# Kernel tuning notes

Hardware: AMD Instinct MI355X
Metric: run time of the kernel (lower is better)

## Reference

```python
import jax, jax.numpy as jnp
import numpy as np

NUM_GRAPHS = 10  # seq_len graphs batched together


def _gat_layer(x, W, al, ar, b, src, dst, n_nodes):
    # x: [N, h_dim]; W: [h_dim, H*D]; al/ar/b: [H, D]
    H, D = al.shape
    feat = (x @ W).reshape(-1, H, D)                      # [N, H, D]
    el = jnp.einsum('nhd,hd->nh', feat, al)               # [N, H]
    er = jnp.einsum('nhd,hd->nh', feat, ar)               # [N, H]
    e = jax.nn.leaky_relu(el[src] + er[dst], 0.2)         # [E, H]
    # edge softmax over incoming edges of each dst node (stable)
    emax = jax.ops.segment_max(e, dst, num_segments=n_nodes)
    emax = jnp.where(jnp.isfinite(emax), emax, 0.0)
    w = jnp.exp(e - emax[dst])                            # [E, H]
    denom = jax.ops.segment_sum(w, dst, num_segments=n_nodes)  # [N, H]
    msg = w[:, :, None] * feat[src]                       # [E, H, D]
    agg = jax.ops.segment_sum(msg, dst, num_segments=n_nodes)  # [N, H, D]
    out = agg / jnp.maximum(denom, 1e-9)[:, :, None] + b
    return out.mean(axis=1)                               # [N, h_dim] (mean over heads)


def setup_inputs() -> dict:
    key = jax.random.key(0)
    ks = jax.random.split(key, 16)
    N, E, V, h, H = 100000, 1000000, 50000, 64, 3
    node_ids = jax.random.randint(ks[0], (N,), 0, V)
    edge_src = jax.random.randint(ks[1], (E,), 0, N)
    edge_dst = jax.random.randint(ks[2], (E,), 0, N)
    node_graph_id = jnp.sort(jax.random.randint(ks[3], (N,), 0, NUM_GRAPHS))
    s = 1.0 / np.sqrt(h)
    return {
        'node_ids': node_ids, 'edge_src': edge_src, 'edge_dst': edge_dst,
        'node_graph_id': node_graph_id,
        'W_embed': jax.random.normal(ks[4], (V, h), jnp.float32),
        'W1': jax.random.normal(ks[5], (h, H * h), jnp.float32) * s,
        'al1': jax.random.normal(ks[6], (H, h), jnp.float32) * s,
        'ar1': jax.random.normal(ks[7], (H, h), jnp.float32) * s,
        'b1': jnp.zeros((H, h), jnp.float32),
        'W2': jax.random.normal(ks[8], (h, H * h), jnp.float32) * s,
        'al2': jax.random.normal(ks[9], (H, h), jnp.float32) * s,
        'ar2': jax.random.normal(ks[10], (H, h), jnp.float32) * s,
        'b2': jnp.zeros((H, h), jnp.float32),
    }


def reference(node_ids, edge_src, edge_dst, node_graph_id, W_embed,
              W1, al1, ar1, b1, W2, al2, ar2, b2):
    n_nodes = node_ids.shape[0]
    h = W_embed[node_ids]                                 # gather embeddings
    h = _gat_layer(h, W1, al1, ar1, b1, edge_src, edge_dst, n_nodes)
    h = _gat_layer(h, W2, al2, ar2, b2, edge_src, edge_dst, n_nodes)
    # dgl.max_nodes: per-graph max pooling over nodes
    global_info = jax.ops.segment_max(h, node_graph_id, num_segments=NUM_GRAPHS)
    return global_info                                    # [NUM_GRAPHS, h_dim]
```

## Files before the change

kernel.cpp:

```cpp
#include <hip/hip_runtime.h>
#include <math.h>


#define HEADS 3
#define HD 64
#define FDIM (HEADS*HD)
#define NCOL 208
#define NUM_GRAPHS 10
#define NPB 32

typedef short bf16x8 __attribute__((ext_vector_type(8)));
typedef float f32x4  __attribute__((ext_vector_type(4)));

__device__ __forceinline__ float bf2f(unsigned short u) {
    return __uint_as_float(((unsigned int)u) << 16);
}
__device__ __forceinline__ unsigned short f2bf(float f) {
    unsigned int u = __float_as_uint(f);
    unsigned int r = (u + 0x7FFFu + ((u >> 16) & 1u)) >> 16;
    return (unsigned short)r;
}

__device__ __forceinline__ int wave_incl_scan(int v, int lane) {
#pragma unroll
    for (int off = 1; off < 64; off <<= 1) {
        int t = __shfl_up(v, off);
        if (lane >= off) v += t;
    }
    return v;
}

__device__ __forceinline__ unsigned int fmap(float f) {
    unsigned int u = __float_as_uint(f);
    return (u & 0x80000000u) ? ~u : (u | 0x80000000u);
}
__device__ __forceinline__ float funmap(unsigned int u) {
    u = (u & 0x80000000u) ? (u & 0x7FFFFFFFu) : ~u;
    return __uint_as_float(u);
}

__global__ void k_prep(const float* __restrict__ W1, const float* __restrict__ al1,
                       const float* __restrict__ ar1,
                       const float* __restrict__ W2, const float* __restrict__ al2,
                       const float* __restrict__ ar2,
                       unsigned short* __restrict__ Wt1, unsigned short* __restrict__ Wt2,
                       unsigned int* __restrict__ gm) {
    int i = blockIdx.x * blockDim.x + threadIdx.x;
    if (i < 2 * NCOL * HD) {
        int l = i / (NCOL * HD), j = i % (NCOL * HD);
        int c = j >> 6, k = j & 63;
        const float* W  = l ? W2  : W1;
        const float* al = l ? al2 : al1;
        const float* ar = l ? ar2 : ar1;
        unsigned short* Wt = l ? Wt2 : Wt1;
        float v = 0.f;
        if (c < FDIM) {
            v = W[k * FDIM + c];
        } else if (c < FDIM + 6) {
            int h = c - FDIM;
            const float* a = (h < 3) ? al : ar;
            int hh = (h < 3) ? h : h - 3;
            float s = 0.f;
            for (int d = 0; d < HD; ++d)
                s += W[k * FDIM + hh * HD + d] * a[hh * HD + d];
            v = s;
        }
        Wt[j] = f2bf(v);
    }
    if (i < NUM_GRAPHS * HD) gm[i] = 0x007FFFFFu;
}

__global__ void k_hist(const int* __restrict__ dst, int* __restrict__ deg, int E) {
    int i = blockIdx.x * blockDim.x + threadIdx.x;
    if (i < E) atomicAdd(&deg[dst[i]], 1);
}

__global__ void k_scan1(const int* __restrict__ deg, int* __restrict__ tmp,
                        int* __restrict__ partials, int N) {
    int t = threadIdx.x, b = blockIdx.x;
    int i = b * 256 + t;
    int v = (i < N) ? deg[i] : 0;
    int lane = t & 63, w = t >> 6;
    int incl = wave_incl_scan(v, lane);
    __shared__ int wsum[4];
    if (lane == 63) wsum[w] = incl;
    __syncthreads();
    int off = 0;
    for (int j = 0; j < w; ++j) off += wsum[j];
    incl += off;
    if (i < N) tmp[i] = incl;
    if (t == 255) partials[b] = incl;
}

__global__ void k_scan2(int* __restrict__ partials, int nb) {
    int t = threadIdx.x;
    int v = (t < nb) ? partials[t] : 0;
    int lane = t & 63, w = t >> 6;
    int incl = wave_incl_scan(v, lane);
    __shared__ int wsum[8];
    if (lane == 63) wsum[w] = incl;
    __syncthreads();
    int off = 0;
    for (int j = 0; j < w; ++j) off += wsum[j];
    incl += off;
    if (t < nb) partials[t] = incl;
}

__global__ void k_scan3(const int* __restrict__ tmp, const int* __restrict__ deg,
                        const int* __restrict__ partials, int* __restrict__ rowptr,
                        int* __restrict__ cur, int N) {
    int i = blockIdx.x * blockDim.x + threadIdx.x;
    if (i >= N) return;
    int b = i >> 8;
    int off = b ? partials[b - 1] : 0;
    int incl = tmp[i] + off;
    rowptr[i + 1] = incl;
    cur[i] = incl - deg[i];
    if (i == 0) rowptr[0] = 0;
}

__global__ void k_scatter(const int* __restrict__ src, const int* __restrict__ dst,
                          int* __restrict__ cur, int* __restrict__ csrc, int E) {
    int i = blockIdx.x * blockDim.x + threadIdx.x;
    if (i >= E) return;
    int pos = atomicAdd(&cur[dst[i]], 1);
    csrc[pos] = src[i];
}

__global__ __launch_bounds__(256) void k_feat_mfma(
        const unsigned short* __restrict__ xbf, const int* __restrict__ ids,
        const float* __restrict__ Wemb, const unsigned short* __restrict__ Wt,
        unsigned short* __restrict__ feat, float4* __restrict__ el4,
        float4* __restrict__ er4, int N) {
    __shared__ unsigned short xs[NPB][72];
    __shared__ unsigned short ls[NPB][200];
    int t = threadIdx.x;
    int lane = t & 63, w = t >> 6;
    int base = blockIdx.x * NPB;

    if (ids) {
        for (int i = t; i < NPB * 16; i += 256) {
            int row = i >> 4, c4 = (i & 15) * 4;
            int n = base + row;
            float4 v = {0.f, 0.f, 0.f, 0.f};
            if (n < N) v = *(const float4*)(Wemb + (size_t)ids[n] * HD + c4);
            unsigned short* dp = &xs[row][c4];
            dp[0] = f2bf(v.x); dp[1] = f2bf(v.y); dp[2] = f2bf(v.z); dp[3] = f2bf(v.w);
        }
    } else {
        for (int i = t; i < NPB * 16; i += 256) {
            int row = i >> 4, c4 = (i & 15) * 4;
            int n = base + row;
            ushort4 v = {0, 0, 0, 0};
            if (n < N) v = *(const ushort4*)(xbf + (size_t)n * HD + c4);
            *(ushort4*)(&xs[row][c4]) = v;
        }
    }

    int ntile = (w == 3) ? 4 : 3;
    bf16x8 bfrag[4][2];
#pragma unroll
    for (int c = 0; c < 4; ++c) {
        if (c >= ntile) break;
#pragma unroll
        for (int kk = 0; kk < 2; ++kk) {
            int coln = (w * 3 + c) * 16 + (lane & 15);
            int k0 = kk * 32 + (lane >> 4) * 8;
            bfrag[c][kk] = *(const bf16x8*)(Wt + (size_t)coln * HD + k0);
        }
    }
    __syncthreads();

    f32x4 acc[2][4];
#pragma unroll
    for (int r = 0; r < 2; ++r)
#pragma unroll
        for (int c = 0; c < 4; ++c) acc[r][c] = (f32x4){0.f, 0.f, 0.f, 0.f};
#pragma unroll
    for (int r = 0; r < 2; ++r)
#pragma unroll
        for (int kk = 0; kk < 2; ++kk) {
            int row = r * 16 + (lane & 15);
            int k0 = kk * 32 + (lane >> 4) * 8;
            bf16x8 a = *(const bf16x8*)(&xs[row][k0]);
#pragma unroll
            for (int c = 0; c < 4; ++c) {
                if (c >= ntile) break;
                acc[r][c] = __builtin_amdgcn_mfma_f32_16x16x32_bf16(a, bfrag[c][kk], acc[r][c], 0, 0, 0);
            }
        }

#pragma unroll
    for (int r = 0; r < 2; ++r)
#pragma unroll
        for (int c = 0; c < 3; ++c) {
            int col = (w * 3 + c) * 16 + (lane & 15);
#pragma unroll
            for (int j = 0; j < 4; ++j) {
                int row = r * 16 + (lane >> 4) * 4 + j;
                ls[row][col] = f2bf(acc[r][c][j]);
            }
        }

    if (w == 3) {
        int col = lane & 15;
        if (col < 6) {
#pragma unroll
            for (int r = 0; r < 2; ++r)
#pragma unroll
                for (int j = 0; j < 4; ++j) {
                    int row = r * 16 + (lane >> 4) * 4 + j;
                    int n = base + row;
                    if (n < N) {
                        float v = acc[r][3][j];
                        if (col < 3) ((float*)&el4[n])[col] = v;
                        else         ((float*)&er4[n])[col - 3] = v;
                    }
                }
        }
    }
    __syncthreads();

    for (int i = t; i < NPB * FDIM / 4; i += 256) {
        int idx = i * 4;
        int row = idx / FDIM, col = idx % FDIM;
        int n = base + row;
        if (n < N)
            *(ushort4*)(feat + (size_t)n * FDIM + col) = *(const ushort4*)(&ls[row][col]);
    }
}

__global__ void k_gather(const int* __restrict__ rowptr, const int* __restrict__ csrc,
                         const float4* __restrict__ el4, const float4* __restrict__ er4,
                         const unsigned short* __restrict__ feat,
                         const float* __restrict__ b,
                         unsigned short* __restrict__ xout, int N) {
    __shared__ float4 stage[4][64];
    int wid = (blockIdx.x * blockDim.x + threadIdx.x) >> 6;
    int lane = threadIdx.x & 63, w = (threadIdx.x >> 6) & 3;
    if (wid >= N) return;
    int beg = rowptr[wid], end = rowptr[wid + 1];
    int deg = end - beg;
    float4 er = er4[wid];
    float acc0 = 0.f, acc1 = 0.f, acc2 = 0.f;
    float ds0 = 0.f, ds1 = 0.f, ds2 = 0.f;
    for (int cb = 0; cb < deg; cb += 64) {
        int nch = min(64, deg - cb);
        if (lane < nch) {
            int s = csrc[beg + cb + lane];
            float4 l = el4[s];
            float e0 = l.x + er.x; e0 = e0 >= 0.f ? e0 : 0.2f * e0;
            float e1 = l.y + er.y; e1 = e1 >= 0.f ? e1 : 0.2f * e1;
            float e2 = l.z + er.z; e2 = e2 >= 0.f ? e2 : 0.2f * e2;
            float4 o;
            o.x = __int_as_float(s);
            o.y = __expf(e0); o.z = __expf(e1); o.w = __expf(e2);
            stage[w][lane] = o;
        }
        __builtin_amdgcn_wave_barrier();
#pragma unroll 4
        for (int j = 0; j < nch; ++j) {
            float4 e = stage[w][j];
            int s = __float_as_int(e.x);
            const unsigned short* frow = feat + (size_t)s * FDIM;
            acc0 = fmaf(e.y, bf2f(frow[lane]), acc0);
            acc1 = fmaf(e.z, bf2f(frow[HD + lane]), acc1);
            acc2 = fmaf(e.w, bf2f(frow[2 * HD + lane]), acc2);
            ds0 += e.y; ds1 += e.z; ds2 += e.w;
        }
        __builtin_amdgcn_wave_barrier();
    }
    float o = (acc0 / fmaxf(ds0, 1e-9f) + b[lane])
            + (acc1 / fmaxf(ds1, 1e-9f) + b[HD + lane])
            + (acc2 / fmaxf(ds2, 1e-9f) + b[2 * HD + lane]);
    xout[(size_t)wid * HD + lane] = f2bf(o * (1.f / 3.f));
}

__global__ void k_gmax(const unsigned short* __restrict__ x, const int* __restrict__ gid,
                       unsigned int* __restrict__ gm, int N) {
    int lane = threadIdx.x;
    int base = blockIdx.x * 64;
    int endn = min(base + 64, N);
    int cur = -1;
    float m = 0.f;
    for (int n = base; n < endn; ++n) {
        int g = gid[n];
        float v = bf2f(x[(size_t)n * HD + lane]);
        if (g != cur) {
            if (cur >= 0) atomicMax(&gm[cur * HD + lane], fmap(m));
            cur = g; m = v;
        } else {
            m = fmaxf(m, v);
        }
    }
    if (cur >= 0) atomicMax(&gm[cur * HD + lane], fmap(m));
}

__global__ void k_gmax_final(const unsigned int* __restrict__ gm, float* __restrict__ out) {
    int i = blockIdx.x * blockDim.x + threadIdx.x;
    if (i < NUM_GRAPHS * HD) out[i] = funmap(gm[i]);
}

extern "C" void kernel_launch(void* const* d_in, const int* in_sizes, int n_in,
                              void* d_out, int out_size, void* d_ws, size_t ws_size,
                              hipStream_t stream) {
    const int*   node_ids = (const int*)d_in[0];
    const int*   edge_src = (const int*)d_in[1];
    const int*   edge_dst = (const int*)d_in[2];
    const int*   gid      = (const int*)d_in[3];
    const float* Wemb     = (const float*)d_in[4];
    const float* W1  = (const float*)d_in[5];
    const float* al1 = (const float*)d_in[6];
    const float* ar1 = (const float*)d_in[7];
    const float* b1  = (const float*)d_in[8];
    const float* W2  = (const float*)d_in[9];
    const float* al2 = (const float*)d_in[10];
    const float* ar2 = (const float*)d_in[11];
    const float* b2  = (const float*)d_in[12];

    int N = in_sizes[0];
    int E = in_sizes[1];

    char* p = (char*)d_ws;
    auto alloc = [&](size_t bytes) {
        char* r = p;
        p += (bytes + 255) & ~(size_t)255;
        return (void*)r;
    };
    int*   deg      = (int*)alloc((size_t)N * 4);
    int*   tmp      = (int*)alloc((size_t)N * 4);
    int*   partials = (int*)alloc(512 * 4);
    int*   rowptr   = (int*)alloc((size_t)(N + 1) * 4);
    int*   cur      = (int*)alloc((size_t)N * 4);
    int*   csrc     = (int*)alloc((size_t)E * 4);
    unsigned short* feat = (unsigned short*)alloc((size_t)N * FDIM * 2);
    unsigned short* Wt1  = (unsigned short*)alloc((size_t)NCOL * HD * 2);
    unsigned short* Wt2  = (unsigned short*)alloc((size_t)NCOL * HD * 2);
    float4* el4     = (float4*)alloc((size_t)N * 16);
    float4* er4     = (float4*)alloc((size_t)N * 16);
    unsigned short* x1b = (unsigned short*)alloc((size_t)N * HD * 2);
    unsigned int* gm = (unsigned int*)alloc(NUM_GRAPHS * HD * 4);
    (void)ws_size;

    int nb = (N + 255) / 256;

    hipMemsetAsync(deg, 0, (size_t)N * 4, stream);
    k_prep<<<dim3((2 * NCOL * HD + 255) / 256), dim3(256), 0, stream>>>(
        W1, al1, ar1, W2, al2, ar2, Wt1, Wt2, gm);
    k_hist<<<dim3((E + 255) / 256), dim3(256), 0, stream>>>(edge_dst, deg, E);
    k_scan1<<<dim3(nb), dim3(256), 0, stream>>>(deg, tmp, partials, N);
    k_scan2<<<dim3(1), dim3(512), 0, stream>>>(partials, nb);
    k_scan3<<<dim3(nb), dim3(256), 0, stream>>>(tmp, deg, partials, rowptr, cur, N);
    k_scatter<<<dim3((E + 255) / 256), dim3(256), 0, stream>>>(edge_src, edge_dst, cur, csrc, E);

    dim3 featGrid((N + NPB - 1) / NPB), featBlk(256);
    dim3 aggGrid((N * 64 + 255) / 256), aggBlk(256);

    k_feat_mfma<<<featGrid, featBlk, 0, stream>>>(nullptr, node_ids, Wemb, Wt1,
                                                  feat, el4, er4, N);
    k_gather<<<aggGrid, aggBlk, 0, stream>>>(rowptr, csrc, el4, er4, feat, b1, x1b, N);

    k_feat_mfma<<<featGrid, featBlk, 0, stream>>>(x1b, nullptr, nullptr, Wt2,
                                                  feat, el4, er4, N);
    k_gather<<<aggGrid, aggBlk, 0, stream>>>(rowptr, csrc, el4, er4, feat, b2, x1b, N);

    k_gmax<<<dim3((N + 63) / 64), dim3(64), 0, stream>>>(x1b, gid, gm, N);
    k_gmax_final<<<dim3(1), dim3(NUM_GRAPHS * HD), 0, stream>>>(gm, (float*)d_out);
}
```

Baseline: 331.6 us.

## Fuse layer-1 feature transform with CSR edge scatter in one interleaved launch

The CSR scatter kernel and the first-layer embedding-gather plus MFMA feature kernel are independent, so they are merged into one launch. Blocks are interleaved 4 feature blocks to 5 scatter blocks per group, so the atomic-heavy scatter and the compute-heavy projection can share the GPU at the same time and one launch boundary goes away. Scatter blocks now reserve the same LDS and register budget as the feature blocks, which may cut occupancy for the scatter part.

```diff
diff --git a/kernel.cpp b/kernel.cpp
--- a/kernel.cpp
+++ b/kernel.cpp
@@ -119,24 +119,16 @@
     if (i == 0) rowptr[0] = 0;
 }
 
-__global__ void k_scatter(const int* __restrict__ src, const int* __restrict__ dst,
-                          int* __restrict__ cur, int* __restrict__ csrc, int E) {
-    int i = blockIdx.x * blockDim.x + threadIdx.x;
-    if (i >= E) return;
-    int pos = atomicAdd(&cur[dst[i]], 1);
-    csrc[pos] = src[i];
-}
-
-__global__ __launch_bounds__(256) void k_feat_mfma(
+__device__ __forceinline__ void feat_body(
         const unsigned short* __restrict__ xbf, const int* __restrict__ ids,
         const float* __restrict__ Wemb, const unsigned short* __restrict__ Wt,
         unsigned short* __restrict__ feat, float4* __restrict__ el4,
-        float4* __restrict__ er4, int N) {
+        float4* __restrict__ er4, int N, int blk) {
     __shared__ unsigned short xs[NPB][72];
     __shared__ unsigned short ls[NPB][200];
     int t = threadIdx.x;
     int lane = t & 63, w = t >> 6;
-    int base = blockIdx.x * NPB;
+    int base = blk * NPB;
 
     if (ids) {
         for (int i = t; i < NPB * 16; i += 256) {
@@ -227,6 +219,36 @@
         int n = base + row;
         if (n < N)
             *(ushort4*)(feat + (size_t)n * FDIM + col) = *(const ushort4*)(&ls[row][col]);
+    }
+}
+
+__global__ __launch_bounds__(256) void k_feat_mfma(
+        const unsigned short* __restrict__ xbf, const int* __restrict__ ids,
+        const float* __restrict__ Wemb, const unsigned short* __restrict__ Wt,
+        unsigned short* __restrict__ feat, float4* __restrict__ el4,
+        float4* __restrict__ er4, int N) {
+    feat_body(xbf, ids, Wemb, Wt, feat, el4, er4, N, blockIdx.x);
+}
+
+__global__ __launch_bounds__(256) void k_feat1_scatter(
+        const int* __restrict__ ids, const float* __restrict__ Wemb,
+        const unsigned short* __restrict__ Wt,
+        unsigned short* __restrict__ feat, float4* __restrict__ el4,
+        float4* __restrict__ er4, int N,
+        const int* __restrict__ src, const int* __restrict__ dst,
+        int* __restrict__ cur, int* __restrict__ csrc, int E) {
+    int g = blockIdx.x / 9, r = blockIdx.x % 9;
+    if (r < 4) {
+        int fb = g * 4 + r;
+        if (fb * NPB < N)
+            feat_body(nullptr, ids, Wemb, Wt, feat, el4, er4, N, fb);
+    } else {
+        int sb = g * 5 + (r - 4);
+        int i = sb * 256 + (int)threadIdx.x;
+        if (i < E) {
+            int pos = atomicAdd(&cur[dst[i]], 1);
+            csrc[pos] = src[i];
+        }
     }
 }
 
@@ -351,13 +373,18 @@
     k_scan1<<<dim3(nb), dim3(256), 0, stream>>>(deg, tmp, partials, N);
     k_scan2<<<dim3(1), dim3(512), 0, stream>>>(partials, nb);
     k_scan3<<<dim3(nb), dim3(256), 0, stream>>>(tmp, deg, partials, rowptr, cur, N);
-    k_scatter<<<dim3((E + 255) / 256), dim3(256), 0, stream>>>(edge_src, edge_dst, cur, csrc, E);
 
     dim3 featGrid((N + NPB - 1) / NPB), featBlk(256);
     dim3 aggGrid((N * 64 + 255) / 256), aggBlk(256);
 
-    k_feat_mfma<<<featGrid, featBlk, 0, stream>>>(nullptr, node_ids, Wemb, Wt1,
-                                                  feat, el4, er4, N);
+    int nf = (N + NPB - 1) / NPB;
+    int ns = (E + 255) / 256;
+    int ngroups = ((nf + 3) / 4 > (ns + 4) / 5) ? (nf + 3) / 4 : (ns + 4) / 5;
+    dim3 fusedGrid(ngroups * 9);
+
+    k_feat1_scatter<<<fusedGrid, featBlk, 0, stream>>>(
+        node_ids, Wemb, Wt1, feat, el4, er4, N,
+        edge_src, edge_dst, cur, csrc, E);
     k_gather<<<aggGrid, aggBlk, 0, stream>>>(rowptr, csrc, el4, er4, feat, b1, x1b, N);
 
     k_feat_mfma<<<featGrid, featBlk, 0, stream>>>(x1b, nullptr, nullptr, Wt2,
```

After: 301.8 us. 9.0% less time.
